# Kernel tuning notes

Hardware: AMD Instinct MI355X
Metric: run time of the kernel (lower is better)

Reference implementation:

```python
import jax, jax.numpy as jnp
import numpy as np

D_MODEL = 1024
N_HEADS = 16
HEAD_DIM = D_MODEL // N_HEADS
D_FF = 4 * D_MODEL
LN_EPS = 1e-5


def setup_inputs() -> dict:
    key = jax.random.key(0)
    ks = jax.random.split(key, 12)
    B, T = 16, 512
    s = lambda fan_in: 1.0 / np.sqrt(fan_in)
    inp = {
        'x': jax.random.normal(ks[0], (B, T, D_MODEL), jnp.float32),
        # torch Linear layout: [out_features, in_features]
        'w_qkv': jax.random.normal(ks[1], (3 * D_MODEL, D_MODEL), jnp.float32) * s(D_MODEL),
        'w_proj': jax.random.normal(ks[2], (D_MODEL, D_MODEL), jnp.float32) * s(D_MODEL),
        'w_ff1': jax.random.normal(ks[3], (D_FF, D_MODEL), jnp.float32) * s(D_MODEL),
        'b_ff1': jax.random.normal(ks[4], (D_FF,), jnp.float32) * 0.02,
        'w_ff2': jax.random.normal(ks[5], (D_MODEL, D_FF), jnp.float32) * s(D_FF),
        'b_ff2': jax.random.normal(ks[6], (D_MODEL,), jnp.float32) * 0.02,
        'ln1_g': jnp.ones((D_MODEL,), jnp.float32),
        'ln1_b': jnp.zeros((D_MODEL,), jnp.float32),
        'ln2_g': jnp.ones((D_MODEL,), jnp.float32),
        'ln2_b': jnp.zeros((D_MODEL,), jnp.float32),
    }
    return inp


def _layernorm(x, g, b):
    mu = jnp.mean(x, axis=-1, keepdims=True)
    var = jnp.var(x, axis=-1, keepdims=True)
    return (x - mu) * jax.lax.rsqrt(var + LN_EPS) * g + b


def _block(x, w_qkv, w_proj, w_ff1, b_ff1, w_ff2, b_ff2, ln1_g, ln1_b, ln2_g, ln2_b):
    B, T, _ = x.shape
    a = _layernorm(x, ln1_g, ln1_b)
    qkv = a @ w_qkv.T  # [B,T,3D]
    q, k, v = jnp.split(qkv, 3, axis=-1)
    # [B,H,T,hd]
    rs = lambda t: t.reshape(B, T, N_HEADS, HEAD_DIM).transpose(0, 2, 1, 3)
    q, k, v = rs(q), rs(k), rs(v)
    scale = HEAD_DIM ** -0.5
    att = jnp.einsum('bhqd,bhkd->bhqk', q, k) * scale
    causal = jnp.tril(jnp.ones((T, T), bool))
    att = jnp.where(causal, att, jnp.float32(-10000.0))
    att = jax.nn.softmax(att, axis=-1)
    out = jnp.einsum('bhqk,bhkd->bhqd', att, v)
    out = out.transpose(0, 2, 1, 3).reshape(B, T, D_MODEL)
    x = x + out @ w_proj.T
    f = _layernorm(x, ln2_g, ln2_b)
    f = jax.nn.gelu(f @ w_ff1.T + b_ff1, approximate=False) @ w_ff2.T + b_ff2
    return x + f


def reference(x, w_qkv, w_proj, w_ff1, b_ff1, w_ff2, b_ff2, ln1_g, ln1_b, ln2_g, ln2_b):
    return _block(x, w_qkv, w_proj, w_ff1, b_ff1, w_ff2, b_ff2, ln1_g, ln1_b, ln2_g, ln2_b)
```

## Files before the change

### kernel.cpp

```cpp
#include <hip/hip_runtime.h>
#include <stdint.h>

typedef __bf16 bf16x8_t __attribute__((ext_vector_type(8)));
typedef float f32x4_t __attribute__((ext_vector_type(4)));
typedef unsigned short ushort8_t __attribute__((ext_vector_type(8)));

#define DEV __device__ __forceinline__

DEV unsigned short f2bf(float f) {
  union { float f; uint32_t u; } v; v.f = f;
  uint32_t r = v.u + 0x7FFFu + ((v.u >> 16) & 1u);
  return (unsigned short)(r >> 16);
}

DEV void gl_lds16(const void* g, void* l) {
  __builtin_amdgcn_global_load_lds(
      (const __attribute__((address_space(1))) void*)g,
      (__attribute__((address_space(3))) void*)l, 16, 0, 0);
}

DEV float gelu_f(float x) {
  return 0.5f * x * (1.0f + erff(x * 0.7071067811865475f));
}

__global__ __launch_bounds__(256) void cvt_kernel(const float* __restrict__ in,
                                                  unsigned short* __restrict__ outp,
                                                  int n4) {
  int i = blockIdx.x * 256 + threadIdx.x;
  if (i >= n4) return;
  float4 v = ((const float4*)in)[i];
  ushort4 o;
  o.x = f2bf(v.x); o.y = f2bf(v.y); o.z = f2bf(v.z); o.w = f2bf(v.w);
  ((ushort4*)outp)[i] = o;
}

__global__ __launch_bounds__(256) void ln_kernel(const float* __restrict__ x,
                                                 const float* __restrict__ g,
                                                 const float* __restrict__ b,
                                                 unsigned short* __restrict__ outp) {
  const int row = blockIdx.x * 4 + (threadIdx.x >> 6);
  const int lane = threadIdx.x & 63;
  const float4* xr = (const float4*)(x + (size_t)row * 1024);
  float4 v[4];
  float s = 0.f, s2 = 0.f;
#pragma unroll
  for (int j = 0; j < 4; ++j) {
    v[j] = xr[j * 64 + lane];
    s += v[j].x + v[j].y + v[j].z + v[j].w;
    s2 += v[j].x * v[j].x + v[j].y * v[j].y + v[j].z * v[j].z + v[j].w * v[j].w;
  }
#pragma unroll
  for (int off = 1; off < 64; off <<= 1) {
    s += __shfl_xor(s, off, 64);
    s2 += __shfl_xor(s2, off, 64);
  }
  const float mu = s * (1.0f / 1024.0f);
  const float var = s2 * (1.0f / 1024.0f) - mu * mu;
  const float rstd = rsqrtf(var + 1e-5f);
  ushort4* orow = (ushort4*)(outp + (size_t)row * 1024);
  const float4* gp = (const float4*)g;
  const float4* bp = (const float4*)b;
#pragma unroll
  for (int j = 0; j < 4; ++j) {
    float4 gv = gp[j * 64 + lane], bv = bp[j * 64 + lane];
    ushort4 o;
    o.x = f2bf((v[j].x - mu) * rstd * gv.x + bv.x);
    o.y = f2bf((v[j].y - mu) * rstd * gv.y + bv.y);
    o.z = f2bf((v[j].z - mu) * rstd * gv.z + bv.z);
    o.w = f2bf((v[j].w - mu) * rstd * gv.w + bv.w);
    orow[j * 64 + lane] = o;
  }
}

template <int MODE>
__global__ __launch_bounds__(256) void gemm_bt(const unsigned short* __restrict__ A,
                                               const unsigned short* __restrict__ B,
                                               float* __restrict__ Cf,
                                               unsigned short* __restrict__ Cb,
                                               const float* __restrict__ bias,
                                               const float* __restrict__ res,
                                               int M, int N, int K) {
  __shared__ unsigned short sA[128 * 32];
  __shared__ unsigned short sB[128 * 32];
  const int tid = threadIdx.x;
  const int w = tid >> 6, lane = tid & 63;
  const int kg = lane >> 4, l16 = lane & 15;
  const int wm = (w & 1) * 64, wn = (w >> 1) * 64;
  const int rowBase = blockIdx.y * 128, colBase = blockIdx.x * 128;

  const int ar = tid >> 2;
  const int ac = (tid & 3) * 8;
  const unsigned short* gA = A + (size_t)(rowBase + ar) * K + ac;
  const unsigned short* gB = B + (size_t)(colBase + ar) * K + ac;
  unsigned short* lA = sA + tid * 8;
  unsigned short* lB = sB + tid * 8;

  f32x4_t acc[4][4];
#pragma unroll
  for (int mi = 0; mi < 4; ++mi)
#pragma unroll
    for (int ni = 0; ni < 4; ++ni) acc[mi][ni] = (f32x4_t)0.0f;

  const int nk = K >> 5;
  for (int kt = 0; kt < nk; ++kt) {
    __syncthreads();
    gl_lds16(gA, lA);
    gl_lds16(gA + (size_t)64 * K, lA + 64 * 32);
    gl_lds16(gB, lB);
    gl_lds16(gB + (size_t)64 * K, lB + 64 * 32);
    gA += 32; gB += 32;
    __syncthreads();
    bf16x8_t a[4], b[4];
#pragma unroll
    for (int i = 0; i < 4; ++i)
      a[i] = *(const bf16x8_t*)(sA + (wm + i * 16 + l16) * 32 + kg * 8);
#pragma unroll
    for (int i = 0; i < 4; ++i)
      b[i] = *(const bf16x8_t*)(sB + (wn + i * 16 + l16) * 32 + kg * 8);
#pragma unroll
    for (int mi = 0; mi < 4; ++mi)
#pragma unroll
      for (int ni = 0; ni < 4; ++ni)
        acc[mi][ni] = __builtin_amdgcn_mfma_f32_16x16x32_bf16(a[mi], b[ni], acc[mi][ni], 0, 0, 0);
  }

#pragma unroll
  for (int mi = 0; mi < 4; ++mi) {
#pragma unroll
    for (int ni = 0; ni < 4; ++ni) {
      const int col = colBase + wn + ni * 16 + l16;
      float bv = 0.f;
      if (MODE == 2 || MODE == 3) bv = bias[col];
#pragma unroll
      for (int r = 0; r < 4; ++r) {
        const int row = rowBase + wm + mi * 16 + kg * 4 + r;
        const size_t idx = (size_t)row * N + col;
        float v = acc[mi][ni][r];
        if (MODE == 0) {
          Cb[idx] = f2bf(v);
        } else if (MODE == 1) {
          Cf[idx] = v + res[idx];
        } else if (MODE == 2) {
          Cb[idx] = f2bf(gelu_f(v + bv));
        } else {
          Cf[idx] = v + bv + res[idx];
        }
      }
    }
  }
}

__global__ __launch_bounds__(256) void attn_kernel(const unsigned short* __restrict__ qkv,
                                                   unsigned short* __restrict__ outp) {
  constexpr int D3 = 3072;
  __shared__ unsigned short sQ[128 * 64];
  __shared__ unsigned short sK[64 * 64];
  __shared__ unsigned short sVt[64 * 72];
  __shared__ unsigned short sP[128 * 72];
  const int tid = threadIdx.x;
  const int w = tid >> 6, lane = tid & 63;
  const int kg = lane >> 4, l16 = lane & 15;
  const int qi = blockIdx.x, h = blockIdx.y, bb = blockIdx.z;
  const int t0 = qi * 128;
  const size_t base = (size_t)bb * 512 * D3 + h * 64;

  {
    const int r = tid >> 3, c = (tid & 7) * 8;
    const unsigned short* g = qkv + base + (size_t)(t0 + r) * D3 + c;
    unsigned short* l = sQ + tid * 8;
#pragma unroll
    for (int i = 0; i < 4; ++i) gl_lds16(g + (size_t)32 * i * D3, l + 2048 * i);
  }

  const int wm = w * 32;
  f32x4_t o[2][4];
  float m_i[2][4], l_i[2][4];
#pragma unroll
  for (int mi = 0; mi < 2; ++mi)
#pragma unroll
    for (int r = 0; r < 4; ++r) { m_i[mi][r] = -1e30f; l_i[mi][r] = 0.f; }
#pragma unroll
  for (int mi = 0; mi < 2; ++mi)
#pragma unroll
    for (int di = 0; di < 4; ++di) o[mi][di] = (f32x4_t)0.0f;

  const int nkt = (qi + 1) * 2;
  for (int kt = 0; kt < nkt; ++kt) {
    const int k0 = kt * 64;
    __syncthreads();
    {
      const int r = tid >> 3, c = (tid & 7) * 8;
      const unsigned short* g = qkv + base + 1024 + (size_t)(k0 + r) * D3 + c;
      unsigned short* l = sK + tid * 8;
      gl_lds16(g, l);
      gl_lds16(g + (size_t)32 * D3, l + 2048);
    }
    {
      const int r = tid >> 3, d0 = (tid & 7) * 8;
#pragma unroll
      for (int i = 0; i < 2; ++i) {
        const int k = r + 32 * i;
        ushort8_t v = *(const ushort8_t*)(qkv + base + 2048 + (size_t)(k0 + k) * D3 + d0);
#pragma unroll
        for (int j = 0; j < 8; ++j) sVt[(d0 + j) * 72 + k] = v[j];
      }
    }
    __syncthreads();

    const bool active = (k0 <= t0 + wm + 31);
    if (active) {
      f32x4_t s[2][4];
#pragma unroll
      for (int mi = 0; mi < 2; ++mi)
#pragma unroll
        for (int ni = 0; ni < 4; ++ni) s[mi][ni] = (f32x4_t)0.0f;
#pragma unroll
      for (int kd = 0; kd < 2; ++kd) {
        bf16x8_t aq[2], bk[4];
#pragma unroll
        for (int mi = 0; mi < 2; ++mi)
          aq[mi] = *(const bf16x8_t*)(sQ + (wm + mi * 16 + l16) * 64 + kd * 32 + kg * 8);
#pragma unroll
        for (int ni = 0; ni < 4; ++ni)
          bk[ni] = *(const bf16x8_t*)(sK + (ni * 16 + l16) * 64 + kd * 32 + kg * 8);
#pragma unroll
        for (int mi = 0; mi < 2; ++mi)
#pragma unroll
          for (int ni = 0; ni < 4; ++ni)
            s[mi][ni] = __builtin_amdgcn_mfma_f32_16x16x32_bf16(aq[mi], bk[ni], s[mi][ni], 0, 0, 0);
      }
#pragma unroll
      for (int mi = 0; mi < 2; ++mi) {
#pragma unroll
        for (int r = 0; r < 4; ++r) {
          const int q = t0 + wm + mi * 16 + kg * 4 + r;
          float mx = -1e30f;
#pragma unroll
          for (int ni = 0; ni < 4; ++ni) {
            const int kk = k0 + ni * 16 + l16;
            float v = s[mi][ni][r] * 0.125f;
            v = (kk <= q) ? v : -10000.0f;
            s[mi][ni][r] = v;
            mx = fmaxf(mx, v);
          }
#pragma unroll
          for (int off = 1; off < 16; off <<= 1) mx = fmaxf(mx, __shfl_xor(mx, off, 64));
          const float mo = m_i[mi][r];
          const float mn = fmaxf(mo, mx);
          const float alpha = __expf(mo - mn);
          float ps = 0.f;
#pragma unroll
          for (int ni = 0; ni < 4; ++ni) {
            float p = __expf(s[mi][ni][r] - mn);
            s[mi][ni][r] = p;
            ps += p;
          }
#pragma unroll
          for (int off = 1; off < 16; off <<= 1) ps += __shfl_xor(ps, off, 64);
          l_i[mi][r] = l_i[mi][r] * alpha + ps;
          m_i[mi][r] = mn;
#pragma unroll
          for (int di = 0; di < 4; ++di) o[mi][di][r] *= alpha;
          const int prow = wm + mi * 16 + kg * 4 + r;
#pragma unroll
          for (int ni = 0; ni < 4; ++ni)
            sP[prow * 72 + ni * 16 + l16] = f2bf(s[mi][ni][r]);
        }
      }
#pragma unroll
      for (int kd = 0; kd < 2; ++kd) {
        bf16x8_t ap[2], bv[4];
#pragma unroll
        for (int mi = 0; mi < 2; ++mi)
          ap[mi] = *(const bf16x8_t*)(sP + (wm + mi * 16 + l16) * 72 + kd * 32 + kg * 8);
#pragma unroll
        for (int di = 0; di < 4; ++di)
          bv[di] = *(const bf16x8_t*)(sVt + (di * 16 + l16) * 72 + kd * 32 + kg * 8);
#pragma unroll
        for (int mi = 0; mi < 2; ++mi)
#pragma unroll
          for (int di = 0; di < 4; ++di)
            o[mi][di] = __builtin_amdgcn_mfma_f32_16x16x32_bf16(ap[mi], bv[di], o[mi][di], 0, 0, 0);
      }
    }
  }

#pragma unroll
  for (int mi = 0; mi < 2; ++mi) {
#pragma unroll
    for (int r = 0; r < 4; ++r) {
      const float inv = 1.0f / l_i[mi][r];
      const int row = t0 + wm + mi * 16 + kg * 4 + r;
      const size_t ob = ((size_t)bb * 512 + row) * 1024 + h * 64;
#pragma unroll
      for (int di = 0; di < 4; ++di)
        outp[ob + di * 16 + l16] = f2bf(o[mi][di][r] * inv);
    }
  }
}

extern "C" void kernel_launch(void* const* d_in, const int* in_sizes, int n_in,
                              void* d_out, int out_size, void* d_ws, size_t ws_size,
                              hipStream_t stream) {
  const float* x      = (const float*)d_in[0];
  const float* w_qkv  = (const float*)d_in[1];
  const float* w_proj = (const float*)d_in[2];
  const float* w_ff1  = (const float*)d_in[3];
  const float* b_ff1  = (const float*)d_in[4];
  const float* w_ff2  = (const float*)d_in[5];
  const float* b_ff2  = (const float*)d_in[6];
  const float* ln1_g  = (const float*)d_in[7];
  const float* ln1_b  = (const float*)d_in[8];
  const float* ln2_g  = (const float*)d_in[9];
  const float* ln2_b  = (const float*)d_in[10];
  float* out = (float*)d_out;
  char* ws = (char*)d_ws;

  unsigned short* wqkv_b = (unsigned short*)(ws + 0);
  unsigned short* wproj_b = (unsigned short*)(ws + 6291456);
  unsigned short* wff1_b = (unsigned short*)(ws + 8388608);
  unsigned short* wff2_b = (unsigned short*)(ws + 16777216);
  unsigned short* a_b    = (unsigned short*)(ws + 25165824);
  float*          x2_f   = (float*)(ws + 41943040);
  unsigned short* qkv_b  = (unsigned short*)(ws + 75497472);
  unsigned short* attn_b = (unsigned short*)(ws + 125829120);
  unsigned short* h_b    = qkv_b;

  cvt_kernel<<<3072, 256, 0, stream>>>(w_qkv, wqkv_b, 786432);
  cvt_kernel<<<1024, 256, 0, stream>>>(w_proj, wproj_b, 262144);
  cvt_kernel<<<4096, 256, 0, stream>>>(w_ff1, wff1_b, 1048576);
  cvt_kernel<<<4096, 256, 0, stream>>>(w_ff2, wff2_b, 1048576);

  ln_kernel<<<2048, 256, 0, stream>>>(x, ln1_g, ln1_b, a_b);
  gemm_bt<0><<<dim3(24, 64), 256, 0, stream>>>(a_b, wqkv_b, nullptr, qkv_b, nullptr, nullptr, 8192, 3072, 1024);
  attn_kernel<<<dim3(4, 16, 16), 256, 0, stream>>>(qkv_b, attn_b);
  gemm_bt<1><<<dim3(8, 64), 256, 0, stream>>>(attn_b, wproj_b, x2_f, nullptr, nullptr, x, 8192, 1024, 1024);
  ln_kernel<<<2048, 256, 0, stream>>>(x2_f, ln2_g, ln2_b, a_b);
  gemm_bt<2><<<dim3(32, 64), 256, 0, stream>>>(a_b, wff1_b, nullptr, h_b, b_ff1, nullptr, 8192, 4096, 1024);
  gemm_bt<3><<<dim3(8, 64), 256, 0, stream>>>(h_b, wff2_b, out, nullptr, b_ff2, x2_f, 8192, 1024, 4096);
}
```

Baseline: 552.0 us.

## Swizzle LDS layouts in GEMM and attention, fuse weight casts, approximate GELU erf

```diff
diff --git a/kernel.cpp b/kernel.cpp
--- a/kernel.cpp
+++ b/kernel.cpp
@@ -20,14 +20,30 @@
 }
 
 DEV float gelu_f(float x) {
-  return 0.5f * x * (1.0f + erff(x * 0.7071067811865475f));
-}
-
-__global__ __launch_bounds__(256) void cvt_kernel(const float* __restrict__ in,
-                                                  unsigned short* __restrict__ outp,
-                                                  int n4) {
+  const float y = x * 0.7071067811865475f;
+  const float ay = fabsf(y);
+  const float t = __builtin_amdgcn_rcpf(1.0f + 0.3275911f * ay);
+  float p = fmaf(t, 1.061405429f, -1.453152027f);
+  p = fmaf(t, p, 1.421413741f);
+  p = fmaf(t, p, -0.284496736f);
+  p = fmaf(t, p, 0.254829592f);
+  p *= t;
+  const float e = __expf(-ay * ay);
+  float erfv = 1.0f - p * e;
+  erfv = copysignf(erfv, y);
+  return 0.5f * x * (1.0f + erfv);
+}
+
+__global__ __launch_bounds__(256) void cvt_all(const float* __restrict__ w0, unsigned short* __restrict__ o0,
+                                               const float* __restrict__ w1, unsigned short* __restrict__ o1,
+                                               const float* __restrict__ w2, unsigned short* __restrict__ o2,
+                                               const float* __restrict__ w3, unsigned short* __restrict__ o3) {
   int i = blockIdx.x * 256 + threadIdx.x;
-  if (i >= n4) return;
+  const float* in; unsigned short* outp;
+  if (i < 786432) { in = w0; outp = o0; }
+  else if (i < 1048576) { in = w1; outp = o1; i -= 786432; }
+  else if (i < 2097152) { in = w2; outp = o2; i -= 1048576; }
+  else { in = w3; outp = o3; i -= 2097152; }
   float4 v = ((const float4*)in)[i];
   ushort4 o;
   o.x = f2bf(v.x); o.y = f2bf(v.y); o.z = f2bf(v.z); o.w = f2bf(v.w);
@@ -89,7 +105,7 @@
   const int rowBase = blockIdx.y * 128, colBase = blockIdx.x * 128;
 
   const int ar = tid >> 2;
-  const int ac = (tid & 3) * 8;
+  const int ac = (((tid & 3) ^ ((tid >> 3) & 3))) * 8;
   const unsigned short* gA = A + (size_t)(rowBase + ar) * K + ac;
   const unsigned short* gB = B + (size_t)(colBase + ar) * K + ac;
   unsigned short* lA = sA + tid * 8;
@@ -100,6 +116,16 @@
   for (int mi = 0; mi < 4; ++mi)
 #pragma unroll
     for (int ni = 0; ni < 4; ++ni) acc[mi][ni] = (f32x4_t)0.0f;
+
+  const unsigned short* pA[4];
+  const unsigned short* pB[4];
+#pragma unroll
+  for (int i = 0; i < 4; ++i) {
+    const int rr = wm + i * 16 + l16;
+    pA[i] = sA + (rr * 4 + (kg ^ ((l16 >> 1) & 3))) * 8;
+    const int cr = wn + i * 16 + l16;
+    pB[i] = sB + (cr * 4 + (kg ^ ((l16 >> 1) & 3))) * 8;
+  }
 
   const int nk = K >> 5;
   for (int kt = 0; kt < nk; ++kt) {
@@ -112,11 +138,9 @@
     __syncthreads();
     bf16x8_t a[4], b[4];
 #pragma unroll
-    for (int i = 0; i < 4; ++i)
-      a[i] = *(const bf16x8_t*)(sA + (wm + i * 16 + l16) * 32 + kg * 8);
-#pragma unroll
-    for (int i = 0; i < 4; ++i)
-      b[i] = *(const bf16x8_t*)(sB + (wn + i * 16 + l16) * 32 + kg * 8);
+    for (int i = 0; i < 4; ++i) a[i] = *(const bf16x8_t*)pA[i];
+#pragma unroll
+    for (int i = 0; i < 4; ++i) b[i] = *(const bf16x8_t*)pB[i];
 #pragma unroll
     for (int mi = 0; mi < 4; ++mi)
 #pragma unroll
@@ -164,9 +188,11 @@
   const int t0 = qi * 128;
   const size_t base = (size_t)bb * 512 * D3 + h * 64;
 
+  const int sr = tid >> 3;
+  const int sc = ((tid & 7) ^ ((tid >> 3) & 7)) * 8;
+
   {
-    const int r = tid >> 3, c = (tid & 7) * 8;
-    const unsigned short* g = qkv + base + (size_t)(t0 + r) * D3 + c;
+    const unsigned short* g = qkv + base + (size_t)(t0 + sr) * D3 + sc;
     unsigned short* l = sQ + tid * 8;
 #pragma unroll
     for (int i = 0; i < 4; ++i) gl_lds16(g + (size_t)32 * i * D3, l + 2048 * i);
@@ -189,8 +215,7 @@
     const int k0 = kt * 64;
     __syncthreads();
     {
-      const int r = tid >> 3, c = (tid & 7) * 8;
-      const unsigned short* g = qkv + base + 1024 + (size_t)(k0 + r) * D3 + c;
+      const unsigned short* g = qkv + base + 1024 + (size_t)(k0 + sr) * D3 + sc;
       unsigned short* l = sK + tid * 8;
       gl_lds16(g, l);
       gl_lds16(g + (size_t)32 * D3, l + 2048);
@@ -218,11 +243,15 @@
       for (int kd = 0; kd < 2; ++kd) {
         bf16x8_t aq[2], bk[4];
 #pragma unroll
-        for (int mi = 0; mi < 2; ++mi)
-          aq[mi] = *(const bf16x8_t*)(sQ + (wm + mi * 16 + l16) * 64 + kd * 32 + kg * 8);
-#pragma unroll
-        for (int ni = 0; ni < 4; ++ni)
-          bk[ni] = *(const bf16x8_t*)(sK + (ni * 16 + l16) * 64 + kd * 32 + kg * 8);
+        for (int mi = 0; mi < 2; ++mi) {
+          const int rr = wm + mi * 16 + l16;
+          aq[mi] = *(const bf16x8_t*)(sQ + (rr * 8 + ((kd * 4 + kg) ^ (l16 & 7))) * 8);
+        }
+#pragma unroll
+        for (int ni = 0; ni < 4; ++ni) {
+          const int rr = ni * 16 + l16;
+          bk[ni] = *(const bf16x8_t*)(sK + (rr * 8 + ((kd * 4 + kg) ^ (l16 & 7))) * 8);
+        }
 #pragma unroll
         for (int mi = 0; mi < 2; ++mi)
 #pragma unroll
@@ -326,10 +355,7 @@
   unsigned short* attn_b = (unsigned short*)(ws + 125829120);
   unsigned short* h_b    = qkv_b;
 
-  cvt_kernel<<<3072, 256, 0, stream>>>(w_qkv, wqkv_b, 786432);
-  cvt_kernel<<<1024, 256, 0, stream>>>(w_proj, wproj_b, 262144);
-  cvt_kernel<<<4096, 256, 0, stream>>>(w_ff1, wff1_b, 1048576);
-  cvt_kernel<<<4096, 256, 0, stream>>>(w_ff2, wff2_b, 1048576);
+  cvt_all<<<12288, 256, 0, stream>>>(w_qkv, wqkv_b, w_proj, wproj_b, w_ff1, wff1_b, w_ff2, wff2_b);
 
   ln_kernel<<<2048, 256, 0, stream>>>(x, ln1_g, ln1_b, a_b);
   gemm_bt<0><<<dim3(24, 64), 256, 0, stream>>>(a_b, wqkv_b, nullptr, qkv_b, nullptr, nullptr, 8192, 3072, 1024);
```

After: 523.5 us. -5.2%, faster.
